# Kernel tuning notes

Measured on AMD Instinct MI355X. Metric: run time of the kernel, lower is better.

Reference implementation:

```python
import jax, jax.numpy as jnp
import numpy as np

R_DIM = 32
D_DIM = 64
N_AGENTS = 16
BATCH = 65536  # num_samples * N_AGENTS = 4096 * 16


def setup_inputs() -> dict:
    key = jax.random.key(0)
    kx, kl, kq, kk, kv, ko = jax.random.split(key, 6)
    x = jax.random.normal(kx, (BATCH, D_DIM, N_AGENTS), dtype=jnp.float32)
    L = jax.random.randint(kl, (BATCH, N_AGENTS, N_AGENTS), 0, 2).astype(jnp.float32)
    Aq = 0.5 * jax.random.normal(kq, (R_DIM, D_DIM), dtype=jnp.float32)
    Ak = 0.5 * jax.random.normal(kk, (R_DIM, D_DIM), dtype=jnp.float32)
    Av = 0.5 * jax.random.normal(kv, (R_DIM, D_DIM), dtype=jnp.float32)
    Ao = 0.5 * jax.random.normal(ko, (1, R_DIM), dtype=jnp.float32)
    return {"x": x, "L": L, "Aq": Aq, "Ak": Ak, "Av": Av, "Ao": Ao}


def reference(x, L, Aq, Ak, Av, Ao):
    B, d, n = x.shape
    S = B // n  # number of samples (x stacks n agents per sample)
    # numNeighbors: count of entries >= 1 in first row of L, plus 1 -> [B,1,1]
    num_neighbors = jnp.sum((L[:, 0, :] >= 1).astype(x.dtype), axis=1).reshape(-1, 1, 1) + 1.0
    # low-rank tanh-activated Q/K/V: [B, r, n]
    Q = jnp.tanh(jnp.einsum("rd,bdn->brn", Aq, x))
    K = jnp.tanh(jnp.einsum("rd,bdn->brn", Ak, x))
    V = jnp.tanh(jnp.einsum("rd,bdn->brn", Av, x))
    # attention over the rank dim r, scaled by sqrt(numNeighbors): [B, r, r]
    scores = jnp.einsum("brn,bsn->brs", Q, K) / jnp.sqrt(num_neighbors)
    attn = jax.nn.softmax(scores, axis=2)
    o = jnp.einsum("brs,bsn->brn", attn, V)  # [B, r, n]
    R = jnp.tanh(jnp.einsum("or,brn->bon", Ao, o))[:, 0, :]  # [B, n]
    R = R.reshape(S, n, n) ** 2
    eye = jnp.eye(n, dtype=R.dtype)
    Rdiag = R * (1.0 - eye)          # R with zeroed diagonal
    Rout = R * eye                    # diagonal of R only
    # Laplacian-like reconstruction: diag gets row-sum of off-diagonals, off-diag negated
    return Rout + eye * jnp.sum(Rdiag, axis=2, keepdims=True) - Rdiag
```

## Files before the change

kernel.cpp:

```cpp
#include <hip/hip_runtime.h>
#include <hip/hip_bf16.h>

#define S_SAMPLES 4096
#define NAG 16

typedef __attribute__((ext_vector_type(8))) short short8;
typedef __attribute__((ext_vector_type(4))) float f32x4;

union F8 { short8 v; unsigned u[4]; };

__device__ __forceinline__ float tanh_fast(float x) {
    float ax = fabsf(x);
    float e  = __expf(-2.0f * ax);
    float t  = (1.0f - e) * __builtin_amdgcn_rcpf(1.0f + e);
    return copysignf(t, x);
}

__device__ __forceinline__ unsigned pk2(float a, float b) {
    float2 f; f.x = a; f.y = b;
    __hip_bfloat162 h = __float22bfloat162_rn(f);
    unsigned r; __builtin_memcpy(&r, &h, 4); return r;
}

__device__ __forceinline__ short bfs(float a) {
    __hip_bfloat16 h = __float2bfloat16(a);
    short r; __builtin_memcpy(&r, &h, 2); return r;
}

__device__ __forceinline__ float4 ld4(const float* p) {
    return *reinterpret_cast<const float4*>(p);
}

#define STR 40

__global__ __launch_bounds__(256, 2) void att_mask_kernel(
    const float* __restrict__ x, const float* __restrict__ L,
    const float* __restrict__ Aq, const float* __restrict__ Ak,
    const float* __restrict__ Av, const float* __restrict__ Ao,
    float* __restrict__ out)
{
    __shared__ alignas(16) short sQ [4][32 * STR];
    __shared__ alignas(16) short sK [4][32 * STR];
    __shared__ alignas(16) short sVt[4][16 * STR];
    __shared__ alignas(16) short sAt[4][32 * STR];
    __shared__ alignas(16) float sRsq[16 * 17];

    const int tid  = threadIdx.x;
    const int lane = tid & 63;
    const int w    = tid >> 6;
    const int c4   = lane & 15;
    const int q    = lane >> 4;
    const int s_idx = blockIdx.x;

    short* qw = sQ[w];  short* kw = sK[w];  short* vtw = sVt[w];  short* atw = sAt[w];

    F8 aF[3][2][2];
    {
        const float* mats[3] = { Aq, Ak, Av };
        #pragma unroll
        for (int m = 0; m < 3; ++m)
            #pragma unroll
            for (int rh = 0; rh < 2; ++rh)
                #pragma unroll
                for (int kb = 0; kb < 2; ++kb) {
                    const float* p = mats[m] + (c4 + 16 * rh) * 64 + 32 * kb + 8 * q;
                    float4 a0 = ld4(p), a1 = ld4(p + 4);
                    aF[m][rh][kb].u[0] = pk2(a0.x, a0.y);
                    aF[m][rh][kb].u[1] = pk2(a0.z, a0.w);
                    aF[m][rh][kb].u[2] = pk2(a1.x, a1.y);
                    aF[m][rh][kb].u[3] = pk2(a1.z, a1.w);
                }
    }
    float4 ao0 = ld4(Ao + 4 * q);
    float4 ao1 = ld4(Ao + 16 + 4 * q);

    {
        int r = lane & 31, hh = lane >> 5;
        uint2 z; z.x = 0; z.y = 0;
        *reinterpret_cast<uint2*>(&qw[r * STR + 16 + 8 * hh]) = z;
        *reinterpret_cast<uint2*>(&qw[r * STR + 20 + 8 * hh]) = z;
        *reinterpret_cast<uint2*>(&kw[r * STR + 16 + 8 * hh]) = z;
        *reinterpret_cast<uint2*>(&kw[r * STR + 20 + 8 * hh]) = z;
    }

    const f32x4 zz = {0.f, 0.f, 0.f, 0.f};

    for (int t = 0; t < 4; ++t) {
        const int i_loc = w * 4 + t;
        const int b     = s_idx * NAG + i_loc;

        float lv = (lane < 16) ? L[(size_t)b * 256 + lane] : 0.0f;
        unsigned long long ball = __ballot(lv >= 1.0f);
        float scale = rsqrtf((float)(__popcll(ball) + 1));

        const float* xb = x + (size_t)b * 1024 + 128 * q + c4;
        float xv[2][8];
        #pragma unroll
        for (int kb = 0; kb < 2; ++kb)
            #pragma unroll
            for (int j = 0; j < 8; ++j)
                xv[kb][j] = xb[512 * kb + 16 * j];
        F8 bx[2];
        #pragma unroll
        for (int kb = 0; kb < 2; ++kb)
            #pragma unroll
            for (int p = 0; p < 4; ++p)
                bx[kb].u[p] = pk2(xv[kb][2 * p], xv[kb][2 * p + 1]);

        f32x4 accQ[2], accK[2], accV[2];
        #pragma unroll
        for (int rh = 0; rh < 2; ++rh) {
            accQ[rh] = __builtin_amdgcn_mfma_f32_16x16x32_bf16(aF[0][rh][0].v, bx[0].v, zz, 0, 0, 0);
            accQ[rh] = __builtin_amdgcn_mfma_f32_16x16x32_bf16(aF[0][rh][1].v, bx[1].v, accQ[rh], 0, 0, 0);
            accK[rh] = __builtin_amdgcn_mfma_f32_16x16x32_bf16(aF[1][rh][0].v, bx[0].v, zz, 0, 0, 0);
            accK[rh] = __builtin_amdgcn_mfma_f32_16x16x32_bf16(aF[1][rh][1].v, bx[1].v, accK[rh], 0, 0, 0);
            accV[rh] = __builtin_amdgcn_mfma_f32_16x16x32_bf16(aF[2][rh][0].v, bx[0].v, zz, 0, 0, 0);
            accV[rh] = __builtin_amdgcn_mfma_f32_16x16x32_bf16(aF[2][rh][1].v, bx[1].v, accV[rh], 0, 0, 0);
        }

        #pragma unroll
        for (int rh = 0; rh < 2; ++rh) {
            float tq[4], tk[4], tv[4];
            #pragma unroll
            for (int r2 = 0; r2 < 4; ++r2) {
                tq[r2] = tanh_fast(accQ[rh][r2]);
                tk[r2] = tanh_fast(accK[rh][r2]);
                tv[r2] = tanh_fast(accV[rh][r2]);
            }
            #pragma unroll
            for (int r2 = 0; r2 < 4; ++r2) {
                int r = 4 * q + r2 + 16 * rh;
                qw[r * STR + c4] = bfs(tq[r2]);
                kw[r * STR + c4] = bfs(tk[r2]);
            }
            uint2 vpk; vpk.x = pk2(tv[0], tv[1]); vpk.y = pk2(tv[2], tv[3]);
            *reinterpret_cast<uint2*>(&vtw[c4 * STR + 4 * q + 16 * rh]) = vpk;
        }
        __syncthreads();

        short8 kfrag[2], qfrag[2];
        #pragma unroll
        for (int hh = 0; hh < 2; ++hh) {
            kfrag[hh] = *reinterpret_cast<const short8*>(&kw[(c4 + 16 * hh) * STR + 8 * q]);
            qfrag[hh] = *reinterpret_cast<const short8*>(&qw[(c4 + 16 * hh) * STR + 8 * q]);
        }
        f32x4 sc[2][2];
        #pragma unroll
        for (int sh = 0; sh < 2; ++sh)
            #pragma unroll
            for (int rh2 = 0; rh2 < 2; ++rh2)
                sc[sh][rh2] = __builtin_amdgcn_mfma_f32_16x16x32_bf16(kfrag[sh], qfrag[rh2], zz, 0, 0, 0);

        #pragma unroll
        for (int rh2 = 0; rh2 < 2; ++rh2) {
            float v[8];
            #pragma unroll
            for (int sh = 0; sh < 2; ++sh)
                #pragma unroll
                for (int r2 = 0; r2 < 4; ++r2)
                    v[sh * 4 + r2] = sc[sh][rh2][r2] * scale;
            float mx = v[0];
            #pragma unroll
            for (int j2 = 1; j2 < 8; ++j2) mx = fmaxf(mx, v[j2]);
            mx = fmaxf(mx, __shfl_xor(mx, 16));
            mx = fmaxf(mx, __shfl_xor(mx, 32));
            float sum = 0.f;
            #pragma unroll
            for (int j2 = 0; j2 < 8; ++j2) { v[j2] = __expf(v[j2] - mx); sum += v[j2]; }
            sum += __shfl_xor(sum, 16);
            sum += __shfl_xor(sum, 32);
            float inv = __builtin_amdgcn_rcpf(sum);
            #pragma unroll
            for (int sh = 0; sh < 2; ++sh)
                #pragma unroll
                for (int r2 = 0; r2 < 4; ++r2)
                    sc[sh][rh2][r2] = v[sh * 4 + r2] * inv;
        }

        #pragma unroll
        for (int rh2 = 0; rh2 < 2; ++rh2)
            #pragma unroll
            for (int sh = 0; sh < 2; ++sh) {
                uint2 ap; ap.x = pk2(sc[sh][rh2][0], sc[sh][rh2][1]);
                ap.y = pk2(sc[sh][rh2][2], sc[sh][rh2][3]);
                *reinterpret_cast<uint2*>(&atw[(c4 + 16 * rh2) * STR + 4 * q + 16 * sh]) = ap;
            }
        __syncthreads();

        short8 vfrag = *reinterpret_cast<const short8*>(&vtw[c4 * STR + 8 * q]);
        f32x4 o[2];
        #pragma unroll
        for (int rh = 0; rh < 2; ++rh) {
            short8 afr = *reinterpret_cast<const short8*>(&atw[(c4 + 16 * rh) * STR + 8 * q]);
            o[rh] = __builtin_amdgcn_mfma_f32_16x16x32_bf16(afr, vfrag, zz, 0, 0, 0);
        }

        float part = 0.f;
        part = fmaf(ao0.x, o[0][0], part); part = fmaf(ao0.y, o[0][1], part);
        part = fmaf(ao0.z, o[0][2], part); part = fmaf(ao0.w, o[0][3], part);
        part = fmaf(ao1.x, o[1][0], part); part = fmaf(ao1.y, o[1][1], part);
        part = fmaf(ao1.z, o[1][2], part); part = fmaf(ao1.w, o[1][3], part);
        part += __shfl_xor(part, 16);
        part += __shfl_xor(part, 32);
        if (lane < 16) {
            float tt = tanh_fast(part);
            sRsq[i_loc * 17 + lane] = tt * tt;
        }
        __syncthreads();
    }

    {
        int i = tid >> 4, j = tid & 15;
        float rij = sRsq[i * 17 + j];
        float srow = 0.0f;
        #pragma unroll
        for (int k = 0; k < 16; ++k) srow += sRsq[i * 17 + k];
        out[(size_t)s_idx * 256 + tid] = (i == j) ? srow : -rij;
    }
}

extern "C" void kernel_launch(void* const* d_in, const int* in_sizes, int n_in,
                              void* d_out, int out_size, void* d_ws, size_t ws_size,
                              hipStream_t stream) {
    const float* x  = (const float*)d_in[0];
    const float* L  = (const float*)d_in[1];
    const float* Aq = (const float*)d_in[2];
    const float* Ak = (const float*)d_in[3];
    const float* Av = (const float*)d_in[4];
    const float* Ao = (const float*)d_in[5];
    float* out = (float*)d_out;

    dim3 grid(S_SAMPLES), block(256);
    hipLaunchKernelGGL(att_mask_kernel, grid, block, 0, stream,
                       x, L, Aq, Ak, Av, Ao, out);
}
```

Measured before the change: 399.2 us.

## Keep attention and V fragments in registers with K16 MFMA, drop per-iteration block barriers

Switches the Q·K and attn·V products to 16x16x16 bf16 MFMA so the softmax output and the tanh(V) values feed the next MFMA straight from registers. This removes the sVt and sAt shared buffers, the zero-padding writes and two of the three __syncthreads per iteration. Only a compiler fence separates the per-wave LDS writes of Q and K from the reads, and a single barrier before the epilogue replaces the per-iteration one. It also unrolls the t-loop, shrinks the LDS stride and raises launch bounds to 3 blocks per SM. The risk is that a compiler-only fence does not order LDS traffic within the wave, and that more register pressure comes with the higher occupancy target.

New measurement: 401.4 us. No clear change (+0.6%).

```diff
diff --git a/kernel.cpp b/kernel.cpp
--- a/kernel.cpp
+++ b/kernel.cpp
@@ -3,11 +3,14 @@
 
 #define S_SAMPLES 4096
 #define NAG 16
+#define STR 36
 
 typedef __attribute__((ext_vector_type(8))) short short8;
+typedef __attribute__((ext_vector_type(4))) short short4v;
 typedef __attribute__((ext_vector_type(4))) float f32x4;
 
 union F8 { short8 v; unsigned u[4]; };
+union F4 { short4v v; unsigned u[2]; };
 
 __device__ __forceinline__ float tanh_fast(float x) {
     float ax = fabsf(x);
@@ -31,18 +34,26 @@
     return *reinterpret_cast<const float4*>(p);
 }
 
-#define STR 40
-
-__global__ __launch_bounds__(256, 2) void att_mask_kernel(
+__device__ __forceinline__ f32x4 mfma_k16(short4v a, short4v b, f32x4 c) {
+#if __has_builtin(__builtin_amdgcn_mfma_f32_16x16x16bf16_1k)
+    return __builtin_amdgcn_mfma_f32_16x16x16bf16_1k(a, b, c, 0, 0, 0);
+#else
+    short8 a8 = { a[0], a[1], a[2], a[3], 0, 0, 0, 0 };
+    short8 b8 = { b[0], b[1], b[2], b[3], 0, 0, 0, 0 };
+    return __builtin_amdgcn_mfma_f32_16x16x32_bf16(a8, b8, c, 0, 0, 0);
+#endif
+}
+
+#define WAVE_FENCE() __asm__ volatile("" ::: "memory")
+
+__global__ __launch_bounds__(256, 3) void att_mask_kernel(
     const float* __restrict__ x, const float* __restrict__ L,
     const float* __restrict__ Aq, const float* __restrict__ Ak,
     const float* __restrict__ Av, const float* __restrict__ Ao,
     float* __restrict__ out)
 {
-    __shared__ alignas(16) short sQ [4][32 * STR];
-    __shared__ alignas(16) short sK [4][32 * STR];
-    __shared__ alignas(16) short sVt[4][16 * STR];
-    __shared__ alignas(16) short sAt[4][32 * STR];
+    __shared__ alignas(16) short sQ[4][32 * STR];
+    __shared__ alignas(16) short sK[4][32 * STR];
     __shared__ alignas(16) float sRsq[16 * 17];
 
     const int tid  = threadIdx.x;
@@ -52,7 +63,8 @@
     const int q    = lane >> 4;
     const int s_idx = blockIdx.x;
 
-    short* qw = sQ[w];  short* kw = sK[w];  short* vtw = sVt[w];  short* atw = sAt[w];
+    short* qw = sQ[w];
+    short* kw = sK[w];
 
     F8 aF[3][2][2];
     {
@@ -74,17 +86,9 @@
     float4 ao0 = ld4(Ao + 4 * q);
     float4 ao1 = ld4(Ao + 16 + 4 * q);
 
-    {
-        int r = lane & 31, hh = lane >> 5;
-        uint2 z; z.x = 0; z.y = 0;
-        *reinterpret_cast<uint2*>(&qw[r * STR + 16 + 8 * hh]) = z;
-        *reinterpret_cast<uint2*>(&qw[r * STR + 20 + 8 * hh]) = z;
-        *reinterpret_cast<uint2*>(&kw[r * STR + 16 + 8 * hh]) = z;
-        *reinterpret_cast<uint2*>(&kw[r * STR + 20 + 8 * hh]) = z;
-    }
-
     const f32x4 zz = {0.f, 0.f, 0.f, 0.f};
 
+    #pragma unroll
     for (int t = 0; t < 4; ++t) {
         const int i_loc = w * 4 + t;
         const int b     = s_idx * NAG + i_loc;
@@ -118,6 +122,8 @@
             accV[rh] = __builtin_amdgcn_mfma_f32_16x16x32_bf16(aF[2][rh][1].v, bx[1].v, accV[rh], 0, 0, 0);
         }
 
+        WAVE_FENCE();
+        F4 vB[2];
         #pragma unroll
         for (int rh = 0; rh < 2; ++rh) {
             float tq[4], tk[4], tv[4];
@@ -133,23 +139,23 @@
                 qw[r * STR + c4] = bfs(tq[r2]);
                 kw[r * STR + c4] = bfs(tk[r2]);
             }
-            uint2 vpk; vpk.x = pk2(tv[0], tv[1]); vpk.y = pk2(tv[2], tv[3]);
-            *reinterpret_cast<uint2*>(&vtw[c4 * STR + 4 * q + 16 * rh]) = vpk;
-        }
-        __syncthreads();
-
-        short8 kfrag[2], qfrag[2];
-        #pragma unroll
-        for (int hh = 0; hh < 2; ++hh) {
-            kfrag[hh] = *reinterpret_cast<const short8*>(&kw[(c4 + 16 * hh) * STR + 8 * q]);
-            qfrag[hh] = *reinterpret_cast<const short8*>(&qw[(c4 + 16 * hh) * STR + 8 * q]);
+            vB[rh].u[0] = pk2(tv[0], tv[1]);
+            vB[rh].u[1] = pk2(tv[2], tv[3]);
+        }
+        WAVE_FENCE();
+
+        short4v kA[2], qB[2];
+        #pragma unroll
+        for (int h = 0; h < 2; ++h) {
+            kA[h] = *reinterpret_cast<const short4v*>(&kw[(c4 + 16 * h) * STR + 4 * q]);
+            qB[h] = *reinterpret_cast<const short4v*>(&qw[(c4 + 16 * h) * STR + 4 * q]);
         }
         f32x4 sc[2][2];
         #pragma unroll
         for (int sh = 0; sh < 2; ++sh)
             #pragma unroll
             for (int rh2 = 0; rh2 < 2; ++rh2)
-                sc[sh][rh2] = __builtin_amdgcn_mfma_f32_16x16x32_bf16(kfrag[sh], qfrag[rh2], zz, 0, 0, 0);
+                sc[sh][rh2] = mfma_k16(kA[sh], qB[rh2], zz);
 
         #pragma unroll
         for (int rh2 = 0; rh2 < 2; ++rh2) {
@@ -177,22 +183,15 @@
                     sc[sh][rh2][r2] = v[sh * 4 + r2] * inv;
         }
 
-        #pragma unroll
-        for (int rh2 = 0; rh2 < 2; ++rh2)
-            #pragma unroll
-            for (int sh = 0; sh < 2; ++sh) {
-                uint2 ap; ap.x = pk2(sc[sh][rh2][0], sc[sh][rh2][1]);
-                ap.y = pk2(sc[sh][rh2][2], sc[sh][rh2][3]);
-                *reinterpret_cast<uint2*>(&atw[(c4 + 16 * rh2) * STR + 4 * q + 16 * sh]) = ap;
-            }
-        __syncthreads();
-
-        short8 vfrag = *reinterpret_cast<const short8*>(&vtw[c4 * STR + 8 * q]);
         f32x4 o[2];
         #pragma unroll
         for (int rh = 0; rh < 2; ++rh) {
-            short8 afr = *reinterpret_cast<const short8*>(&atw[(c4 + 16 * rh) * STR + 8 * q]);
-            o[rh] = __builtin_amdgcn_mfma_f32_16x16x32_bf16(afr, vfrag, zz, 0, 0, 0);
+            F4 aA0, aA1;
+            aA0.u[0] = pk2(sc[0][rh][0], sc[0][rh][1]);
+            aA0.u[1] = pk2(sc[0][rh][2], sc[0][rh][3]);
+            aA1.u[0] = pk2(sc[1][rh][0], sc[1][rh][1]);
+            aA1.u[1] = pk2(sc[1][rh][2], sc[1][rh][3]);
+            o[rh] = mfma_k16(aA1.v, vB[1].v, mfma_k16(aA0.v, vB[0].v, zz));
         }
 
         float part = 0.f;
@@ -206,8 +205,9 @@
             float tt = tanh_fast(part);
             sRsq[i_loc * 17 + lane] = tt * tt;
         }
-        __syncthreads();
     }
+
+    __syncthreads();
 
     {
         int i = tid >> 4, j = tid & 15;
```
